# Kernel tuning notes

Measured on AMD Instinct MI355X. Metric: run time of the kernel, lower is better.

Reference implementation:

```python
import jax, jax.numpy as jnp
import numpy as np

N_NODES = 50000
N_EDGES = 800000
R = 3          # relations
D_IN = 96
D_HID = 96
D_OUT = 64


def setup_inputs() -> dict:
    key = jax.random.key(0)
    ks = jax.random.split(key, 10)
    s_in = 1.0 / np.sqrt(D_IN)
    s_hid = 1.0 / np.sqrt(D_HID)
    return {
        "x": jax.random.normal(ks[0], (N_NODES, D_IN), jnp.float32),
        "src": jax.random.randint(ks[1], (R, N_EDGES), 0, N_NODES, jnp.int32),
        "dst": jax.random.randint(ks[2], (R, N_EDGES), 0, N_NODES, jnp.int32),
        "Ws1": jax.random.normal(ks[3], (R, D_IN, D_HID), jnp.float32) * s_in,
        "Wn1": jax.random.normal(ks[4], (R, D_IN, D_HID), jnp.float32) * s_in,
        "b1": jnp.zeros((R, D_HID), jnp.float32),
        "Ws2": jax.random.normal(ks[5], (R, D_HID, D_OUT), jnp.float32) * s_hid,
        "Wn2": jax.random.normal(ks[6], (R, D_HID, D_OUT), jnp.float32) * s_hid,
        "b2": jnp.zeros((R, D_OUT), jnp.float32),
    }


def reference(x, src, dst, Ws1, Wn1, b1, Ws2, Wn2, b2):
    N = x.shape[0]
    # in-degree per relation, clamped to 1 (DGL zero-in-degree convention)
    deg = jax.vmap(lambda d: jax.ops.segment_sum(
        jnp.ones(d.shape[0], x.dtype), d, num_segments=N))(dst)        # [R, N]
    inv_deg = (1.0 / jnp.maximum(deg, 1.0))[..., None]                 # [R, N, 1]

    def sage_layer(h, Ws, Wn, b):
        # gather src feats, mean-aggregate onto dst, per relation
        neigh = jax.vmap(lambda s, d: jax.ops.segment_sum(
            h[s], d, num_segments=N))(src, dst) * inv_deg              # [R, N, Din]
        out = jnp.tanh(
            jnp.einsum('nd,rdh->rnh', h, Ws)
            + jnp.einsum('rnd,rdh->rnh', neigh, Wn)
            + b[:, None, :])                                           # [R, N, H]
        return out.mean(axis=0)  # HeteroGraphConv aggregate='mean'

    h1 = sage_layer(x, Ws1, Wn1, b1)
    return sage_layer(h1, Ws2, Wn2, b2)
```

## Files before the change

### kernel.cpp

```cpp
#include <hip/hip_runtime.h>
#include <hip/hip_bf16.h>

constexpr int NN   = 50000;
constexpr int NE   = 800000;
constexpr int NR   = 3;
constexpr int DIN  = 96;
constexpr int DH   = 96;
constexpr int DOUT = 64;
constexpr int SLOT = 48;
constexpr int ZROW = NN;

constexpr float QS_X   = 127.0f / 5.5f;
constexpr float STEP_X = 5.5f / 127.0f;
constexpr float STEP_H = 1.0f / 127.0f;

constexpr int NBUCK   = 196;
constexpr int LCAP    = 56;
constexpr int P1B     = 256;
constexpr int CHUNK   = NE / P1B;
constexpr int BSTRIDE = 3200;
constexpr int LSTRIDE = 200;

constexpr int SCAT_BLKS = NR * P1B;
constexpr int CONV_BLKS = (NN * 96 + 4095) / 4096;
constexpr int WT_ELEMS  = 2 * NR * DIN * DH + 2 * NR * DH * DOUT;
constexpr int WT_BLKS   = (WT_ELEMS + 511) / 512;
constexpr int PREP_GRID = SCAT_BLKS + CONV_BLKS + WT_BLKS;

constexpr int LPAD = 104;

typedef __attribute__((ext_vector_type(8))) short bf16x8;
typedef __attribute__((ext_vector_type(4))) float f32x4;
typedef __attribute__((ext_vector_type(4))) unsigned int uint4v;

__device__ __forceinline__ unsigned short f2b(float f) {
    unsigned int u = __float_as_uint(f);
    u += 0x7fffu + ((u >> 16) & 1u);
    return (unsigned short)(u >> 16);
}
__device__ __forceinline__ unsigned int pack2(float lo, float hi) {
    return (unsigned int)f2b(lo) | ((unsigned int)f2b(hi) << 16);
}
__device__ __forceinline__ unsigned int q8u(float f, float s) {
    int v = (int)lrintf(f * s);
    v = v < -127 ? -127 : (v > 127 ? 127 : v);
    return (unsigned int)(v + 128);
}
__device__ __forceinline__ float fast_tanh(float x) {
    x = fminf(fmaxf(x, -30.0f), 30.0f);
    float e = exp2f(x * 2.8853900817779268f);
    return (e - 1.0f) * __builtin_amdgcn_rcpf(e + 1.0f);
}

struct __align__(4) U3 { unsigned int x, y, z; };

__global__ __launch_bounds__(512)
void prep_kernel(const int* __restrict__ src,
                 const int* __restrict__ dst,
                 unsigned int* __restrict__ gbuck,
                 int* __restrict__ glofs,
                 const float* __restrict__ x,
                 unsigned short* __restrict__ xb,
                 unsigned char* __restrict__ xq,
                 unsigned short* __restrict__ h1b,
                 unsigned char* __restrict__ h1q,
                 const float* __restrict__ Ws1, const float* __restrict__ Wn1,
                 const float* __restrict__ Ws2, const float* __restrict__ Wn2,
                 unsigned short* __restrict__ wt)
{
    __shared__ unsigned int lbuf[NBUCK][LCAP];
    __shared__ int lcnt[NBUCK];
    __shared__ int sa[256], sb[256];
    __shared__ int lofs[NBUCK + 1];

    const int bid = blockIdx.x;
    const int tid = threadIdx.x;

    if (bid < SCAT_BLKS) {
        const int r = bid >> 8, c = bid & 255;
        for (int i = tid; i < NBUCK; i += 512) lcnt[i] = 0;
        __syncthreads();

        const int* sr = src + (size_t)r * NE + (size_t)c * CHUNK;
        const int* dr = dst + (size_t)r * NE + (size_t)c * CHUNK;
        for (int i = tid; i < CHUNK; i += 512) {
            int d = dr[i];
            int s = sr[i];
            int b = d >> 8;
            int pos = atomicAdd(&lcnt[b], 1);
            if (pos < LCAP)
                lbuf[b][pos] = ((unsigned int)(d & 255) << 16) | (unsigned int)s;
        }
        __syncthreads();

        if (tid < 256)
            sa[tid] = (tid < NBUCK) ? min(lcnt[tid], LCAP) : 0;
        __syncthreads();
        int* cur = sa; int* nxt = sb;
        for (int st = 1; st < 256; st <<= 1) {
            if (tid < 256) {
                int v = cur[tid];
                if (tid >= st) v += cur[tid - st];
                nxt[tid] = v;
            }
            __syncthreads();
            int* t2 = cur; cur = nxt; nxt = t2;
        }
        if (tid == 0) lofs[0] = 0;
        if (tid < NBUCK) lofs[tid + 1] = cur[tid];
        __syncthreads();

        if (tid < NBUCK + 1) glofs[(size_t)bid * LSTRIDE + tid] = lofs[tid];

        const int w = tid >> 6, l = tid & 63;
        unsigned int* gb = gbuck + (size_t)bid * BSTRIDE;
        for (int b = w; b < NBUCK; b += 8) {
            int cnt = min(lcnt[b], LCAP);
            if (l < cnt) gb[lofs[b] + l] = lbuf[b][l];
        }
    } else if (bid < SCAT_BLKS + CONV_BLKS) {
        const int rb = bid - SCAT_BLKS;
        if (rb == 0) {
            if (tid < 48) {
                reinterpret_cast<unsigned int*>(xb  + (size_t)ZROW * 96)[tid] = 0u;
            } else if (tid >= 64 && tid < 112) {
                reinterpret_cast<unsigned int*>(h1b + (size_t)ZROW * 96)[tid - 64] = 0u;
            } else if (tid >= 128 && tid < 152) {
                reinterpret_cast<unsigned int*>(xq  + (size_t)ZROW * 96)[tid - 128] = 0x80808080u;
            } else if (tid >= 192 && tid < 216) {
                reinterpret_cast<unsigned int*>(h1q + (size_t)ZROW * 96)[tid - 192] = 0x80808080u;
            }
        }
        int i = (rb * 512 + tid) * 8;
        if (i < NN * 96) {
            float4 a = *reinterpret_cast<const float4*>(x + i);
            float4 b = *reinterpret_cast<const float4*>(x + i + 4);
            uint4 o;
            o.x = pack2(a.x, a.y);
            o.y = pack2(a.z, a.w);
            o.z = pack2(b.x, b.y);
            o.w = pack2(b.z, b.w);
            *reinterpret_cast<uint4*>(xb + i) = o;
            unsigned int qlo = q8u(a.x, QS_X) | (q8u(a.y, QS_X) << 8)
                             | (q8u(a.z, QS_X) << 16) | (q8u(a.w, QS_X) << 24);
            unsigned int qhi = q8u(b.x, QS_X) | (q8u(b.y, QS_X) << 8)
                             | (q8u(b.z, QS_X) << 16) | (q8u(b.w, QS_X) << 24);
            unsigned int* q = reinterpret_cast<unsigned int*>(xq + i);
            q[0] = qlo;
            q[1] = qhi;
        }
    } else {
        int g = (bid - SCAT_BLKS - CONV_BLKS) * 512 + tid;
        if (g < WT_ELEMS) {
            constexpr int SZ1 = NR * DIN * DH;
            constexpr int SZ2 = NR * DH * DOUT;
            const float* in;
            int idx, KD, ND;
            if (g < SZ1)                { in = Ws1; idx = g;                 KD = DIN; ND = DH; }
            else if (g < 2 * SZ1)       { in = Wn1; idx = g - SZ1;           KD = DIN; ND = DH; }
            else if (g < 2 * SZ1 + SZ2) { in = Ws2; idx = g - 2 * SZ1;       KD = DH;  ND = DOUT; }
            else                        { in = Wn2; idx = g - 2 * SZ1 - SZ2; KD = DH;  ND = DOUT; }
            int k = idx % KD;
            int rn = idx / KD;
            int n = rn % ND;
            int r = rn / ND;
            wt[g] = f2b(in[((size_t)r * KD + k) * ND + n]);
        }
    }
}

__global__ __launch_bounds__(512)
void bin_build_kernel(const unsigned int* __restrict__ gbuck,
                      const int* __restrict__ glofs,
                      unsigned short* __restrict__ slots,
                      int* __restrict__ deg)
{
    __shared__ unsigned short lslot[256][SLOT];
    __shared__ int lcnt[256];

    const int rb = blockIdx.x;
    const int r  = rb / NBUCK, b = rb - r * NBUCK;
    const int nbase = b * 256;
    int nb = NN - nbase; if (nb > 256) nb = 256;
    const int tid = threadIdx.x;

    unsigned int* ls32i = reinterpret_cast<unsigned int*>(&lslot[0][0]);
    for (int i = tid; i < 256 * SLOT / 2; i += 512) ls32i[i] = 0xC350C350u;
    for (int i = tid; i < 256; i += 512) lcnt[i] = 0;
    __syncthreads();

    const int blk  = tid >> 1;
    const int half = tid & 1;
    const int gblk = r * P1B + blk;
    int o0 = glofs[(size_t)gblk * LSTRIDE + b];
    int o1 = glofs[(size_t)gblk * LSTRIDE + b + 1];
    const unsigned int* run = gbuck + (size_t)gblk * BSTRIDE + o0;
    int cnt = o1 - o0;
    for (int i = half; i < cnt; i += 2) {
        unsigned int e = run[i];
        int nl = e >> 16;
        int pos = atomicAdd(&lcnt[nl], 1);
        if (pos < SLOT) lslot[nl][pos] = (unsigned short)(e & 0xffffu);
    }
    __syncthreads();

    for (int j = tid; j < nb; j += 512) deg[r * NN + nbase + j] = lcnt[j];

    const unsigned int* ls32 = reinterpret_cast<const unsigned int*>(&lslot[0][0]);
    unsigned int* gs32 = reinterpret_cast<unsigned int*>(
        slots + ((size_t)r * NN + nbase) * SLOT);
    const int tot = nb * (SLOT / 2);
    for (int i = tid; i < tot; i += 512) gs32[i] = ls32[i];
}

__global__ __launch_bounds__(256)
void agg_q8_kernel(const unsigned char* __restrict__ Hq,
                   const unsigned short* __restrict__ slots,
                   const int* __restrict__ deg,
                   unsigned int* __restrict__ aggb,
                   float step)
{
    int gid = blockIdx.x * 256 + threadIdx.x;
    int grp = gid >> 3, t = gid & 7;
    if (grp >= NR * NN) return;
    const uint4v* sl4 = reinterpret_cast<const uint4v*>(slots + (size_t)grp * SLOT);
    int e = deg[grp];
    if (e > SLOT) e = SLOT;

    uint4v iv0 = __builtin_nontemporal_load(sl4 + 0);
    uint4v iv1 = __builtin_nontemporal_load(sl4 + 1);
    uint4v iv2 = __builtin_nontemporal_load(sl4 + 2);
    uint4v iv3 = __builtin_nontemporal_load(sl4 + 3);

    const unsigned char* Tb = Hq + 12 * t;
    unsigned int l0 = 0, h0 = 0, l1 = 0, h1 = 0, l2 = 0, h2 = 0;
    const unsigned int M = 0x00FF00FFu;

#define DO8Q(V)                                                                \
    {                                                                          \
        unsigned int i0 = (V).x & 0xffffu, i1 = (V).x >> 16;                   \
        unsigned int i2 = (V).y & 0xffffu, i3 = (V).y >> 16;                   \
        unsigned int i4 = (V).z & 0xffffu, i5 = (V).z >> 16;                   \
        unsigned int i6 = (V).w & 0xffffu, i7 = (V).w >> 16;                   \
        U3 g0 = *reinterpret_cast<const U3*>(Tb + (size_t)i0 * 96);            \
        U3 g1 = *reinterpret_cast<const U3*>(Tb + (size_t)i1 * 96);            \
        U3 g2 = *reinterpret_cast<const U3*>(Tb + (size_t)i2 * 96);            \
        U3 g3 = *reinterpret_cast<const U3*>(Tb + (size_t)i3 * 96);            \
        U3 g4 = *reinterpret_cast<const U3*>(Tb + (size_t)i4 * 96);            \
        U3 g5 = *reinterpret_cast<const U3*>(Tb + (size_t)i5 * 96);            \
        U3 g6 = *reinterpret_cast<const U3*>(Tb + (size_t)i6 * 96);            \
        U3 g7 = *reinterpret_cast<const U3*>(Tb + (size_t)i7 * 96);            \
        l0 += g0.x & M; h0 += (g0.x >> 8) & M;                                 \
        l1 += g0.y & M; h1 += (g0.y >> 8) & M;                                 \
        l2 += g0.z & M; h2 += (g0.z >> 8) & M;                                 \
        l0 += g1.x & M; h0 += (g1.x >> 8) & M;                                 \
        l1 += g1.y & M; h1 += (g1.y >> 8) & M;                                 \
        l2 += g1.z & M; h2 += (g1.z >> 8) & M;                                 \
        l0 += g2.x & M; h0 += (g2.x >> 8) & M;                                 \
        l1 += g2.y & M; h1 += (g2.y >> 8) & M;                                 \
        l2 += g2.z & M; h2 += (g2.z >> 8) & M;                                 \
        l0 += g3.x & M; h0 += (g3.x >> 8) & M;                                 \
        l1 += g3.y & M; h1 += (g3.y >> 8) & M;                                 \
        l2 += g3.z & M; h2 += (g3.z >> 8) & M;                                 \
        l0 += g4.x & M; h0 += (g4.x >> 8) & M;                                 \
        l1 += g4.y & M; h1 += (g4.y >> 8) & M;                                 \
        l2 += g4.z & M; h2 += (g4.z >> 8) & M;                                 \
        l0 += g5.x & M; h0 += (g5.x >> 8) & M;                                 \
        l1 += g5.y & M; h1 += (g5.y >> 8) & M;                                 \
        l2 += g5.z & M; h2 += (g5.z >> 8) & M;                                 \
        l0 += g6.x & M; h0 += (g6.x >> 8) & M;                                 \
        l1 += g6.y & M; h1 += (g6.y >> 8) & M;                                 \
        l2 += g6.z & M; h2 += (g6.z >> 8) & M;                                 \
        l0 += g7.x & M; h0 += (g7.x >> 8) & M;                                 \
        l1 += g7.y & M; h1 += (g7.y >> 8) & M;                                 \
        l2 += g7.z & M; h2 += (g7.z >> 8) & M;                                 \
    }

    int nb8 = (e + 7) >> 3;
    if (nb8 > 0) DO8Q(iv0);
    if (nb8 > 1) DO8Q(iv1);
    if (nb8 > 2) DO8Q(iv2);
    if (nb8 > 3) DO8Q(iv3);
    for (int i = 32; i < e; i += 8) {
        uint4v v = __builtin_nontemporal_load(sl4 + (i >> 3));
        DO8Q(v);
    }
#undef DO8Q

    const int bias = 128 * 8 * nb8;
    const float inv = step / (float)(e > 0 ? e : 1);
    float f0  = (float)((int)(l0 & 0xFFFFu) - bias) * inv;
    float f1  = (float)((int)(h0 & 0xFFFFu) - bias) * inv;
    float f2  = (float)((int)(l0 >> 16)     - bias) * inv;
    float f3  = (float)((int)(h0 >> 16)     - bias) * inv;
    float f4  = (float)((int)(l1 & 0xFFFFu) - bias) * inv;
    float f5  = (float)((int)(h1 & 0xFFFFu) - bias) * inv;
    float f6  = (float)((int)(l1 >> 16)     - bias) * inv;
    float f7  = (float)((int)(h1 >> 16)     - bias) * inv;
    float f8  = (float)((int)(l2 & 0xFFFFu) - bias) * inv;
    float f9  = (float)((int)(h2 & 0xFFFFu) - bias) * inv;
    float f10 = (float)((int)(l2 >> 16)     - bias) * inv;
    float f11 = (float)((int)(h2 >> 16)     - bias) * inv;

    unsigned int* o = aggb + (size_t)grp * 48 + t * 6;
    o[0] = pack2(f0, f1);
    o[1] = pack2(f2, f3);
    o[2] = pack2(f4, f5);
    o[3] = pack2(f6, f7);
    o[4] = pack2(f8, f9);
    o[5] = pack2(f10, f11);
}

template <int NOUT, bool OUT16>
__global__ __launch_bounds__(256)
void mfma_layer_kernel(const unsigned short* __restrict__ Hb,
                       const unsigned short* __restrict__ aggb,
                       const unsigned short* __restrict__ Wts,
                       const unsigned short* __restrict__ Wtn,
                       const float* __restrict__ bias,
                       unsigned short* __restrict__ o16,
                       unsigned char* __restrict__ oq8,
                       float* __restrict__ o32)
{
    __shared__ unsigned short lds_s[NOUT * LPAD];
    __shared__ unsigned short lds_n[NOUT * LPAD];

    const int tid  = threadIdx.x;
    const int w    = tid >> 6;
    const int l    = tid & 63;
    const int n0   = blockIdx.x * 64 + w * 16;
    const int arow = l & 15, asel = l >> 4;
    int na = n0 + arow;
    if (na > NN - 1) na = NN - 1;

    bf16x8 ax[3], ag[NR][3];
    {
        const unsigned short* xr = Hb + (size_t)na * 96 + asel * 8;
        #pragma unroll
        for (int kb = 0; kb < 3; ++kb)
            ax[kb] = *reinterpret_cast<const bf16x8*>(xr + kb * 32);
        #pragma unroll
        for (int r = 0; r < NR; ++r) {
            const unsigned short* gr = aggb + ((size_t)r * NN + na) * 96 + asel * 8;
            #pragma unroll
            for (int kb = 0; kb < 3; ++kb)
                ag[r][kb] = *reinterpret_cast<const bf16x8*>(gr + kb * 32);
        }
    }

    constexpr int NC = NOUT / 16;
    float res[NC][4];
    #pragma unroll
    for (int c = 0; c < NC; ++c)
        #pragma unroll
        for (int j = 0; j < 4; ++j) res[c][j] = 0.f;

    unsigned int* ls32 = reinterpret_cast<unsigned int*>(lds_s);
    unsigned int* ln32 = reinterpret_cast<unsigned int*>(lds_n);

    for (int r = 0; r < NR; ++r) {
        if (r > 0) __syncthreads();
        const unsigned int* srcs = reinterpret_cast<const unsigned int*>(
            Wts + (size_t)r * NOUT * 96);
        const unsigned int* srcn = reinterpret_cast<const unsigned int*>(
            Wtn + (size_t)r * NOUT * 96);
        constexpr int NDW = NOUT * 48;
        for (int i = tid; i < NDW; i += 256) {
            int row = i / 48, c2 = i - row * 48;
            ls32[row * (LPAD / 2) + c2] = srcs[i];
            ln32[row * (LPAD / 2) + c2] = srcn[i];
        }
        __syncthreads();

        #pragma unroll
        for (int c = 0; c < NC; ++c) {
            const int col = c * 16 + arow;
            const unsigned short* bs = lds_s + (size_t)col * LPAD + asel * 8;
            const unsigned short* bn = lds_n + (size_t)col * LPAD + asel * 8;
            f32x4 acc = (f32x4){0.f, 0.f, 0.f, 0.f};
            #pragma unroll
            for (int kb = 0; kb < 3; ++kb) {
                acc = __builtin_amdgcn_mfma_f32_16x16x32_bf16(
                    ax[kb], *reinterpret_cast<const bf16x8*>(bs + kb * 32), acc, 0, 0, 0);
                acc = __builtin_amdgcn_mfma_f32_16x16x32_bf16(
                    ag[r][kb], *reinterpret_cast<const bf16x8*>(bn + kb * 32), acc, 0, 0, 0);
            }
            const float bb = bias[r * NOUT + col];
            #pragma unroll
            for (int j = 0; j < 4; ++j)
                res[c][j] += fast_tanh(acc[j] + bb);
        }
    }

    const float third = 1.0f / 3.0f;
    #pragma unroll
    for (int c = 0; c < NC; ++c) {
        const int col = c * 16 + arow;
        #pragma unroll
        for (int j = 0; j < 4; ++j) {
            int node = n0 + asel * 4 + j;
            if (node < NN) {
                float v = res[c][j] * third;
                if (OUT16) {
                    o16[(size_t)node * 96 + col] = f2b(v);
                    oq8[(size_t)node * 96 + col] = (unsigned char)q8u(v, 127.0f);
                } else {
                    o32[(size_t)node * DOUT + col] = v;
                }
            }
        }
    }
}

extern "C" void kernel_launch(void* const* d_in, const int* in_sizes, int n_in,
                              void* d_out, int out_size, void* d_ws, size_t ws_size,
                              hipStream_t stream)
{
    const float* x   = (const float*)d_in[0];
    const int*   src = (const int*)d_in[1];
    const int*   dst = (const int*)d_in[2];
    const float* Ws1 = (const float*)d_in[3];
    const float* Wn1 = (const float*)d_in[4];
    const float* b1  = (const float*)d_in[5];
    const float* Ws2 = (const float*)d_in[6];
    const float* Wn2 = (const float*)d_in[7];
    const float* b2  = (const float*)d_in[8];
    float* out = (float*)d_out;

    char* ws = (char*)d_ws;
    size_t o = 0;
    auto alloc = [&](size_t bytes) {
        size_t p = o;
        o += (bytes + 255) & ~(size_t)255;
        return p;
    };
    int* deg = (int*)(ws + alloc((size_t)NR * NN * 4));
    unsigned short* slots = (unsigned short*)(ws + alloc((size_t)NR * NN * SLOT * 2));
    unsigned short* xb = (unsigned short*)(ws + alloc((size_t)(NN + 1) * 96 * 2));
    unsigned char* xq = (unsigned char*)(ws + alloc((size_t)(NN + 1) * 96));
    unsigned short* h1b = (unsigned short*)(ws + alloc((size_t)(NN + 1) * 96 * 2));
    unsigned char* h1q = (unsigned char*)(ws + alloc((size_t)(NN + 1) * 96));
    char* aggregion = ws + alloc((size_t)NR * NN * 96 * 2);
    unsigned short* wt = (unsigned short*)(ws + alloc((size_t)WT_ELEMS * 2));
    unsigned short* wt1s = wt;
    unsigned short* wt1n = wt1s + NR * DIN * DH;
    unsigned short* wt2s = wt1n + NR * DIN * DH;
    unsigned short* wt2n = wt2s + NR * DH * DOUT;

    unsigned int* gbuck = (unsigned int*)aggregion;
    int* glofs = (int*)(aggregion + (size_t)NR * P1B * BSTRIDE * 4);
    unsigned short* aggb = (unsigned short*)aggregion;

    prep_kernel<<<PREP_GRID, 512, 0, stream>>>(
        src, dst, gbuck, glofs, x, xb, xq, h1b, h1q, Ws1, Wn1, Ws2, Wn2, wt);
    bin_build_kernel<<<NR * NBUCK, 512, 0, stream>>>(gbuck, glofs, slots, deg);

    constexpr int AGG_GRID  = (NR * NN * 8 + 255) / 256;
    constexpr int NBLKN     = (NN + 63) / 64;

    agg_q8_kernel<<<AGG_GRID, 256, 0, stream>>>(
        xq, slots, deg, (unsigned int*)aggb, STEP_X);
    mfma_layer_kernel<DH, true><<<NBLKN, 256, 0, stream>>>(
        xb, aggb, wt1s, wt1n, b1, h1b, h1q, (float*)nullptr);

    agg_q8_kernel<<<AGG_GRID, 256, 0, stream>>>(
        h1q, slots, deg, (unsigned int*)aggb, STEP_H);
    mfma_layer_kernel<DOUT, false><<<NBLKN, 256, 0, stream>>>(
        h1b, aggb, wt2s, wt2n, b2, (unsigned short*)nullptr, (unsigned char*)nullptr, out);
}
```

Before: 173.3 us.

## Split int8 feature tables into 64/32-column slabs and aggregate in two passes

Stores the quantized node features as two separate arrays (first 64 columns and last 32 columns) and runs the neighbor aggregation kernel twice, once per slab, writing into the respective parts of the bf16 aggregate buffer. The intent is to shrink the per-pass gather working set so it fits better in cache and to use naturally aligned 8-byte/4-byte gather loads instead of 12-byte ones. It costs rereading the edge slots and degrees twice per layer and adds extra kernel launches.

```diff
diff --git a/kernel.cpp b/kernel.cpp
--- a/kernel.cpp
+++ b/kernel.cpp
@@ -52,8 +52,6 @@
     return (e - 1.0f) * __builtin_amdgcn_rcpf(e + 1.0f);
 }
 
-struct __align__(4) U3 { unsigned int x, y, z; };
-
 __global__ __launch_bounds__(512)
 void prep_kernel(const int* __restrict__ src,
                  const int* __restrict__ dst,
@@ -61,9 +59,11 @@
                  int* __restrict__ glofs,
                  const float* __restrict__ x,
                  unsigned short* __restrict__ xb,
-                 unsigned char* __restrict__ xq,
+                 unsigned char* __restrict__ xqA,
+                 unsigned char* __restrict__ xqB,
                  unsigned short* __restrict__ h1b,
-                 unsigned char* __restrict__ h1q,
+                 unsigned char* __restrict__ h1qA,
+                 unsigned char* __restrict__ h1qB,
                  const float* __restrict__ Ws1, const float* __restrict__ Wn1,
                  const float* __restrict__ Ws2, const float* __restrict__ Wn2,
                  unsigned short* __restrict__ wt)
@@ -125,14 +125,19 @@
                 reinterpret_cast<unsigned int*>(xb  + (size_t)ZROW * 96)[tid] = 0u;
             } else if (tid >= 64 && tid < 112) {
                 reinterpret_cast<unsigned int*>(h1b + (size_t)ZROW * 96)[tid - 64] = 0u;
-            } else if (tid >= 128 && tid < 152) {
-                reinterpret_cast<unsigned int*>(xq  + (size_t)ZROW * 96)[tid - 128] = 0x80808080u;
-            } else if (tid >= 192 && tid < 216) {
-                reinterpret_cast<unsigned int*>(h1q + (size_t)ZROW * 96)[tid - 192] = 0x80808080u;
+            } else if (tid >= 128 && tid < 144) {
+                reinterpret_cast<unsigned int*>(xqA + (size_t)ZROW * 64)[tid - 128] = 0x80808080u;
+            } else if (tid >= 160 && tid < 168) {
+                reinterpret_cast<unsigned int*>(xqB + (size_t)ZROW * 32)[tid - 160] = 0x80808080u;
+            } else if (tid >= 192 && tid < 208) {
+                reinterpret_cast<unsigned int*>(h1qA + (size_t)ZROW * 64)[tid - 192] = 0x80808080u;
+            } else if (tid >= 224 && tid < 232) {
+                reinterpret_cast<unsigned int*>(h1qB + (size_t)ZROW * 32)[tid - 224] = 0x80808080u;
             }
         }
         int i = (rb * 512 + tid) * 8;
         if (i < NN * 96) {
+            int n = i / 96, d = i - n * 96;
             float4 a = *reinterpret_cast<const float4*>(x + i);
             float4 b = *reinterpret_cast<const float4*>(x + i + 4);
             uint4 o;
@@ -141,13 +146,15 @@
             o.z = pack2(b.x, b.y);
             o.w = pack2(b.z, b.w);
             *reinterpret_cast<uint4*>(xb + i) = o;
-            unsigned int qlo = q8u(a.x, QS_X) | (q8u(a.y, QS_X) << 8)
-                             | (q8u(a.z, QS_X) << 16) | (q8u(a.w, QS_X) << 24);
-            unsigned int qhi = q8u(b.x, QS_X) | (q8u(b.y, QS_X) << 8)
-                             | (q8u(b.z, QS_X) << 16) | (q8u(b.w, QS_X) << 24);
-            unsigned int* q = reinterpret_cast<unsigned int*>(xq + i);
-            q[0] = qlo;
-            q[1] = qhi;
+            uint2 q;
+            q.x = q8u(a.x, QS_X) | (q8u(a.y, QS_X) << 8)
+                | (q8u(a.z, QS_X) << 16) | (q8u(a.w, QS_X) << 24);
+            q.y = q8u(b.x, QS_X) | (q8u(b.y, QS_X) << 8)
+                | (q8u(b.z, QS_X) << 16) | (q8u(b.w, QS_X) << 24);
+            if (d < 64)
+                *reinterpret_cast<uint2*>(xqA + (size_t)n * 64 + d) = q;
+            else
+                *reinterpret_cast<uint2*>(xqB + (size_t)n * 32 + (d - 64)) = q;
         }
     } else {
         int g = (bid - SCAT_BLKS - CONV_BLKS) * 512 + tid;
@@ -213,6 +220,7 @@
     for (int i = tid; i < tot; i += 512) gs32[i] = ls32[i];
 }
 
+template <bool HIGH>
 __global__ __launch_bounds__(256)
 void agg_q8_kernel(const unsigned char* __restrict__ Hq,
                    const unsigned short* __restrict__ slots,
@@ -232,83 +240,100 @@
     uint4v iv2 = __builtin_nontemporal_load(sl4 + 2);
     uint4v iv3 = __builtin_nontemporal_load(sl4 + 3);
 
-    const unsigned char* Tb = Hq + 12 * t;
-    unsigned int l0 = 0, h0 = 0, l1 = 0, h1 = 0, l2 = 0, h2 = 0;
     const unsigned int M = 0x00FF00FFu;
-
-#define DO8Q(V)                                                                \
+    unsigned int l0 = 0, h0 = 0, l1 = 0, h1 = 0;
+
+    if (!HIGH) {
+        const unsigned char* Tb = Hq + 8 * t;
+#define DO8A(V)                                                                \
     {                                                                          \
         unsigned int i0 = (V).x & 0xffffu, i1 = (V).x >> 16;                   \
         unsigned int i2 = (V).y & 0xffffu, i3 = (V).y >> 16;                   \
         unsigned int i4 = (V).z & 0xffffu, i5 = (V).z >> 16;                   \
         unsigned int i6 = (V).w & 0xffffu, i7 = (V).w >> 16;                   \
-        U3 g0 = *reinterpret_cast<const U3*>(Tb + (size_t)i0 * 96);            \
-        U3 g1 = *reinterpret_cast<const U3*>(Tb + (size_t)i1 * 96);            \
-        U3 g2 = *reinterpret_cast<const U3*>(Tb + (size_t)i2 * 96);            \
-        U3 g3 = *reinterpret_cast<const U3*>(Tb + (size_t)i3 * 96);            \
-        U3 g4 = *reinterpret_cast<const U3*>(Tb + (size_t)i4 * 96);            \
-        U3 g5 = *reinterpret_cast<const U3*>(Tb + (size_t)i5 * 96);            \
-        U3 g6 = *reinterpret_cast<const U3*>(Tb + (size_t)i6 * 96);            \
-        U3 g7 = *reinterpret_cast<const U3*>(Tb + (size_t)i7 * 96);            \
-        l0 += g0.x & M; h0 += (g0.x >> 8) & M;                                 \
-        l1 += g0.y & M; h1 += (g0.y >> 8) & M;                                 \
-        l2 += g0.z & M; h2 += (g0.z >> 8) & M;                                 \
-        l0 += g1.x & M; h0 += (g1.x >> 8) & M;                                 \
-        l1 += g1.y & M; h1 += (g1.y >> 8) & M;                                 \
-        l2 += g1.z & M; h2 += (g1.z >> 8) & M;                                 \
-        l0 += g2.x & M; h0 += (g2.x >> 8) & M;                                 \
-        l1 += g2.y & M; h1 += (g2.y >> 8) & M;                                 \
-        l2 += g2.z & M; h2 += (g2.z >> 8) & M;                                 \
-        l0 += g3.x & M; h0 += (g3.x >> 8) & M;                                 \
-        l1 += g3.y & M; h1 += (g3.y >> 8) & M;                                 \
-        l2 += g3.z & M; h2 += (g3.z >> 8) & M;                                 \
-        l0 += g4.x & M; h0 += (g4.x >> 8) & M;                                 \
-        l1 += g4.y & M; h1 += (g4.y >> 8) & M;                                 \
-        l2 += g4.z & M; h2 += (g4.z >> 8) & M;                                 \
-        l0 += g5.x & M; h0 += (g5.x >> 8) & M;                                 \
-        l1 += g5.y & M; h1 += (g5.y >> 8) & M;                                 \
-        l2 += g5.z & M; h2 += (g5.z >> 8) & M;                                 \
-        l0 += g6.x & M; h0 += (g6.x >> 8) & M;                                 \
-        l1 += g6.y & M; h1 += (g6.y >> 8) & M;                                 \
-        l2 += g6.z & M; h2 += (g6.z >> 8) & M;                                 \
-        l0 += g7.x & M; h0 += (g7.x >> 8) & M;                                 \
-        l1 += g7.y & M; h1 += (g7.y >> 8) & M;                                 \
-        l2 += g7.z & M; h2 += (g7.z >> 8) & M;                                 \
-    }
-
-    int nb8 = (e + 7) >> 3;
-    if (nb8 > 0) DO8Q(iv0);
-    if (nb8 > 1) DO8Q(iv1);
-    if (nb8 > 2) DO8Q(iv2);
-    if (nb8 > 3) DO8Q(iv3);
-    for (int i = 32; i < e; i += 8) {
-        uint4v v = __builtin_nontemporal_load(sl4 + (i >> 3));
-        DO8Q(v);
-    }
-#undef DO8Q
-
-    const int bias = 128 * 8 * nb8;
-    const float inv = step / (float)(e > 0 ? e : 1);
-    float f0  = (float)((int)(l0 & 0xFFFFu) - bias) * inv;
-    float f1  = (float)((int)(h0 & 0xFFFFu) - bias) * inv;
-    float f2  = (float)((int)(l0 >> 16)     - bias) * inv;
-    float f3  = (float)((int)(h0 >> 16)     - bias) * inv;
-    float f4  = (float)((int)(l1 & 0xFFFFu) - bias) * inv;
-    float f5  = (float)((int)(h1 & 0xFFFFu) - bias) * inv;
-    float f6  = (float)((int)(l1 >> 16)     - bias) * inv;
-    float f7  = (float)((int)(h1 >> 16)     - bias) * inv;
-    float f8  = (float)((int)(l2 & 0xFFFFu) - bias) * inv;
-    float f9  = (float)((int)(h2 & 0xFFFFu) - bias) * inv;
-    float f10 = (float)((int)(l2 >> 16)     - bias) * inv;
-    float f11 = (float)((int)(h2 >> 16)     - bias) * inv;
-
-    unsigned int* o = aggb + (size_t)grp * 48 + t * 6;
-    o[0] = pack2(f0, f1);
-    o[1] = pack2(f2, f3);
-    o[2] = pack2(f4, f5);
-    o[3] = pack2(f6, f7);
-    o[4] = pack2(f8, f9);
-    o[5] = pack2(f10, f11);
+        uint2 g0 = *reinterpret_cast<const uint2*>(Tb + (size_t)i0 * 64);      \
+        uint2 g1 = *reinterpret_cast<const uint2*>(Tb + (size_t)i1 * 64);      \
+        uint2 g2 = *reinterpret_cast<const uint2*>(Tb + (size_t)i2 * 64);      \
+        uint2 g3 = *reinterpret_cast<const uint2*>(Tb + (size_t)i3 * 64);      \
+        uint2 g4 = *reinterpret_cast<const uint2*>(Tb + (size_t)i4 * 64);      \
+        uint2 g5 = *reinterpret_cast<const uint2*>(Tb + (size_t)i5 * 64);      \
+        uint2 g6 = *reinterpret_cast<const uint2*>(Tb + (size_t)i6 * 64);      \
+        uint2 g7 = *reinterpret_cast<const uint2*>(Tb + (size_t)i7 * 64);      \
+        l0 += g0.x & M; h0 += (g0.x >> 8) & M; l1 += g0.y & M; h1 += (g0.y >> 8) & M; \
+        l0 += g1.x & M; h0 += (g1.x >> 8) & M; l1 += g1.y & M; h1 += (g1.y >> 8) & M; \
+        l0 += g2.x & M; h0 += (g2.x >> 8) & M; l1 += g2.y & M; h1 += (g2.y >> 8) & M; \
+        l0 += g3.x & M; h0 += (g3.x >> 8) & M; l1 += g3.y & M; h1 += (g3.y >> 8) & M; \
+        l0 += g4.x & M; h0 += (g4.x >> 8) & M; l1 += g4.y & M; h1 += (g4.y >> 8) & M; \
+        l0 += g5.x & M; h0 += (g5.x >> 8) & M; l1 += g5.y & M; h1 += (g5.y >> 8) & M; \
+        l0 += g6.x & M; h0 += (g6.x >> 8) & M; l1 += g6.y & M; h1 += (g6.y >> 8) & M; \
+        l0 += g7.x & M; h0 += (g7.x >> 8) & M; l1 += g7.y & M; h1 += (g7.y >> 8) & M; \
+    }
+        int nb8 = (e + 7) >> 3;
+        if (nb8 > 0) DO8A(iv0);
+        if (nb8 > 1) DO8A(iv1);
+        if (nb8 > 2) DO8A(iv2);
+        if (nb8 > 3) DO8A(iv3);
+        for (int i = 32; i < e; i += 8) {
+            uint4v v = __builtin_nontemporal_load(sl4 + (i >> 3));
+            DO8A(v);
+        }
+#undef DO8A
+        const int bias = 128 * 8 * nb8;
+        const float inv = step / (float)(e > 0 ? e : 1);
+        uint4 o;
+        o.x = pack2((float)((int)(l0 & 0xFFFFu) - bias) * inv,
+                    (float)((int)(h0 & 0xFFFFu) - bias) * inv);
+        o.y = pack2((float)((int)(l0 >> 16) - bias) * inv,
+                    (float)((int)(h0 >> 16) - bias) * inv);
+        o.z = pack2((float)((int)(l1 & 0xFFFFu) - bias) * inv,
+                    (float)((int)(h1 & 0xFFFFu) - bias) * inv);
+        o.w = pack2((float)((int)(l1 >> 16) - bias) * inv,
+                    (float)((int)(h1 >> 16) - bias) * inv);
+        *reinterpret_cast<uint4*>(aggb + (size_t)grp * 48 + t * 4) = o;
+    } else {
+        const unsigned char* Tb = Hq + 4 * t;
+#define DO8B(V)                                                                \
+    {                                                                          \
+        unsigned int i0 = (V).x & 0xffffu, i1 = (V).x >> 16;                   \
+        unsigned int i2 = (V).y & 0xffffu, i3 = (V).y >> 16;                   \
+        unsigned int i4 = (V).z & 0xffffu, i5 = (V).z >> 16;                   \
+        unsigned int i6 = (V).w & 0xffffu, i7 = (V).w >> 16;                   \
+        unsigned int g0 = *reinterpret_cast<const unsigned int*>(Tb + (size_t)i0 * 32); \
+        unsigned int g1 = *reinterpret_cast<const unsigned int*>(Tb + (size_t)i1 * 32); \
+        unsigned int g2 = *reinterpret_cast<const unsigned int*>(Tb + (size_t)i2 * 32); \
+        unsigned int g3 = *reinterpret_cast<const unsigned int*>(Tb + (size_t)i3 * 32); \
+        unsigned int g4 = *reinterpret_cast<const unsigned int*>(Tb + (size_t)i4 * 32); \
+        unsigned int g5 = *reinterpret_cast<const unsigned int*>(Tb + (size_t)i5 * 32); \
+        unsigned int g6 = *reinterpret_cast<const unsigned int*>(Tb + (size_t)i6 * 32); \
+        unsigned int g7 = *reinterpret_cast<const unsigned int*>(Tb + (size_t)i7 * 32); \
+        l0 += g0 & M; h0 += (g0 >> 8) & M;                                     \
+        l0 += g1 & M; h0 += (g1 >> 8) & M;                                     \
+        l0 += g2 & M; h0 += (g2 >> 8) & M;                                     \
+        l0 += g3 & M; h0 += (g3 >> 8) & M;                                     \
+        l0 += g4 & M; h0 += (g4 >> 8) & M;                                     \
+        l0 += g5 & M; h0 += (g5 >> 8) & M;                                     \
+        l0 += g6 & M; h0 += (g6 >> 8) & M;                                     \
+        l0 += g7 & M; h0 += (g7 >> 8) & M;                                     \
+    }
+        int nb8 = (e + 7) >> 3;
+        if (nb8 > 0) DO8B(iv0);
+        if (nb8 > 1) DO8B(iv1);
+        if (nb8 > 2) DO8B(iv2);
+        if (nb8 > 3) DO8B(iv3);
+        for (int i = 32; i < e; i += 8) {
+            uint4v v = __builtin_nontemporal_load(sl4 + (i >> 3));
+            DO8B(v);
+        }
+#undef DO8B
+        const int bias = 128 * 8 * nb8;
+        const float inv = step / (float)(e > 0 ? e : 1);
+        uint2 o;
+        o.x = pack2((float)((int)(l0 & 0xFFFFu) - bias) * inv,
+                    (float)((int)(h0 & 0xFFFFu) - bias) * inv);
+        o.y = pack2((float)((int)(l0 >> 16) - bias) * inv,
+                    (float)((int)(h0 >> 16) - bias) * inv);
+        *reinterpret_cast<uint2*>(aggb + (size_t)grp * 48 + 32 + t * 2) = o;
+    }
 }
 
 template <int NOUT, bool OUT16>
@@ -319,7 +344,8 @@
                        const unsigned short* __restrict__ Wtn,
                        const float* __restrict__ bias,
                        unsigned short* __restrict__ o16,
-                       unsigned char* __restrict__ oq8,
+                       unsigned char* __restrict__ oq8A,
+                       unsigned char* __restrict__ oq8B,
                        float* __restrict__ o32)
 {
     __shared__ unsigned short lds_s[NOUT * LPAD];
@@ -403,7 +429,9 @@
                 float v = res[c][j] * third;
                 if (OUT16) {
                     o16[(size_t)node * 96 + col] = f2b(v);
-                    oq8[(size_t)node * 96 + col] = (unsigned char)q8u(v, 127.0f);
+                    unsigned char qv = (unsigned char)q8u(v, 127.0f);
+                    if (col < 64) oq8A[(size_t)node * 64 + col] = qv;
+                    else          oq8B[(size_t)node * 32 + (col - 64)] = qv;
                 } else {
                     o32[(size_t)node * DOUT + col] = v;
                 }
@@ -437,9 +465,11 @@
     int* deg = (int*)(ws + alloc((size_t)NR * NN * 4));
     unsigned short* slots = (unsigned short*)(ws + alloc((size_t)NR * NN * SLOT * 2));
     unsigned short* xb = (unsigned short*)(ws + alloc((size_t)(NN + 1) * 96 * 2));
-    unsigned char* xq = (unsigned char*)(ws + alloc((size_t)(NN + 1) * 96));
+    unsigned char* xqA = (unsigned char*)(ws + alloc((size_t)(NN + 1) * 64));
+    unsigned char* xqB = (unsigned char*)(ws + alloc((size_t)(NN + 1) * 32));
     unsigned short* h1b = (unsigned short*)(ws + alloc((size_t)(NN + 1) * 96 * 2));
-    unsigned char* h1q = (unsigned char*)(ws + alloc((size_t)(NN + 1) * 96));
+    unsigned char* h1qA = (unsigned char*)(ws + alloc((size_t)(NN + 1) * 64));
+    unsigned char* h1qB = (unsigned char*)(ws + alloc((size_t)(NN + 1) * 32));
     char* aggregion = ws + alloc((size_t)NR * NN * 96 * 2);
     unsigned short* wt = (unsigned short*)(ws + alloc((size_t)WT_ELEMS * 2));
     unsigned short* wt1s = wt;
@@ -452,19 +482,25 @@
     unsigned short* aggb = (unsigned short*)aggregion;
 
     prep_kernel<<<PREP_GRID, 512, 0, stream>>>(
-        src, dst, gbuck, glofs, x, xb, xq, h1b, h1q, Ws1, Wn1, Ws2, Wn2, wt);
+        src, dst, gbuck, glofs, x, xb, xqA, xqB, h1b, h1qA, h1qB,
+        Ws1, Wn1, Ws2, Wn2, wt);
     bin_build_kernel<<<NR * NBUCK, 512, 0, stream>>>(gbuck, glofs, slots, deg);
 
-    constexpr int AGG_GRID  = (NR * NN * 8 + 255) / 256;
-    constexpr int NBLKN     = (NN + 63) / 64;
-
-    agg_q8_kernel<<<AGG_GRID, 256, 0, stream>>>(
-        xq, slots, deg, (unsigned int*)aggb, STEP_X);
+    constexpr int AGG_GRID = (NR * NN * 8 + 255) / 256;
+    constexpr int NBLKN    = (NN + 63) / 64;
+
+    agg_q8_kernel<false><<<AGG_GRID, 256, 0, stream>>>(
+        xqA, slots, deg, (unsigned int*)aggb, STEP_X);
+    agg_q8_kernel<true><<<AGG_GRID, 256, 0, stream>>>(
+        xqB, slots, deg, (unsigned int*)aggb, STEP_X);
     mfma_layer_kernel<DH, true><<<NBLKN, 256, 0, stream>>>(
-        xb, aggb, wt1s, wt1n, b1, h1b, h1q, (float*)nullptr);
-
-    agg_q8_kernel<<<AGG_GRID, 256, 0, stream>>>(
-        h1q, slots, deg, (unsigned int*)aggb, STEP_H);
+        xb, aggb, wt1s, wt1n, b1, h1b, h1qA, h1qB, (float*)nullptr);
+
+    agg_q8_kernel<false><<<AGG_GRID, 256, 0, stream>>>(
+        h1qA, slots, deg, (unsigned int*)aggb, STEP_H);
+    agg_q8_kernel<true><<<AGG_GRID, 256, 0, stream>>>(
+        h1qB, slots, deg, (unsigned int*)aggb, STEP_H);
     mfma_layer_kernel<DOUT, false><<<NBLKN, 256, 0, stream>>>(
-        h1b, aggb, wt2s, wt2n, b2, (unsigned short*)nullptr, (unsigned char*)nullptr, out);
-}
+        h1b, aggb, wt2s, wt2n, b2,
+        (unsigned short*)nullptr, (unsigned char*)nullptr, (unsigned char*)nullptr, out);
+}
```

After: 199.1 us. +14.9%, slower.
